# Optimization experiments

Measured on AMD Instinct MI355X. Metric: run time of the kernel, lower is better.

Reference implementation:

```python
import jax, jax.numpy as jnp
import numpy as np

N_NODES = 50000
N_EDGES = 600000
IN_C = 128
OUT_C = 128
N_REL = 8


def setup_inputs() -> dict:
    key = jax.random.key(0)
    k1, k2, k3, k4 = jax.random.split(key, 4)
    x = jax.random.normal(k1, (N_NODES, IN_C), dtype=jnp.float32)
    edge_index = jax.random.randint(k2, (2, N_EDGES), 0, N_NODES, dtype=jnp.int64)
    edge_type = jax.random.randint(k3, (N_EDGES,), 0, N_REL, dtype=jnp.int64)
    weight = jax.random.normal(k4, (N_REL, IN_C, OUT_C), dtype=jnp.float32)
    bias = jnp.zeros((OUT_C,), dtype=jnp.float32)
    return {"x": x, "edge_index": edge_index, "edge_type": edge_type,
            "weight": weight, "bias": bias}


def reference(x, edge_index, edge_type, weight, bias):
    # x: [N, in], edge_index: [2, E] (src, dst), edge_type: [E]
    # weight: [R, in, out], bias: [out]
    N = x.shape[0]
    src = edge_index[0]
    dst = edge_index[1]
    out = jnp.zeros((N, weight.shape[2]), dtype=x.dtype)
    for r in range(weight.shape[0]):
        rel_mask = (edge_type == r).astype(x.dtype)  # [E]
        transformed = x @ weight[r]                  # [N, out]
        msgs = transformed[src] * rel_mask[:, None]  # [E, out]
        sums = jax.ops.segment_sum(msgs, dst, num_segments=N)        # [N, out]
        counts = jax.ops.segment_sum(rel_mask, dst, num_segments=N)  # [N]
        mean = jnp.where(counts[:, None] > 0,
                         sums / jnp.maximum(counts, 1.0)[:, None],
                         0.0)
        out = out + mean
    return out + bias
```

## Files before the change

### kernel.cpp

```cpp
#include <hip/hip_runtime.h>
#include <hip/hip_bf16.h>


#define C128 128
#define BR 16

typedef __attribute__((ext_vector_type(8))) short short8;
typedef __attribute__((ext_vector_type(4))) float f32x4;

__device__ __forceinline__ float bf16u_f32(unsigned short u) {
    union { unsigned int i; float f; } c;
    c.i = ((unsigned int)u) << 16;
    return c.f;
}


__global__ __launch_bounds__(256) void pre_kernel(const int* __restrict__ ei,
                                                  const int* __restrict__ et,
                                                  unsigned* __restrict__ cursor,
                                                  const float* __restrict__ W,
                                                  __hip_bfloat16* __restrict__ WbT,
                                                  const float* __restrict__ x,
                                                  __hip_bfloat16* __restrict__ xb,
                                                  int n_edges, int n_nodes,
                                                  int hblk, int wblk, int wtot, int xt8) {
    int bid = blockIdx.x;
    if (bid < hblk) {
        int e = bid * 256 + threadIdx.x;
        if (e < n_edges)
            atomicAdd(&cursor[(size_t)et[e] * n_nodes + ei[n_edges + e]], 1u);
    } else if (bid < hblk + wblk) {
        int i = (bid - hblk) * 256 + threadIdx.x;
        if (i < wtot) {
            int r = i >> 14, k = (i >> 7) & 127, n = i & 127;
            int kt = k >> 5, cg = (k >> 3) & 3, j = k & 7;
            int nt = n >> 4, l16 = n & 15;
            int pos = ((((r * 4 + kt) * 8 + nt) * 4 + cg) * 16 + l16) * 8 + j;
            WbT[pos] = __float2bfloat16(W[i]);
        }
    } else {
        int i = (bid - hblk - wblk) * 256 + threadIdx.x;
        if (i < xt8) {
            const float4* src = reinterpret_cast<const float4*>(x + (size_t)i * 8);
            float4 v0 = src[0], v1 = src[1];
            short8 o;
            o[0] = (short)__bfloat16_as_ushort(__float2bfloat16(v0.x));
            o[1] = (short)__bfloat16_as_ushort(__float2bfloat16(v0.y));
            o[2] = (short)__bfloat16_as_ushort(__float2bfloat16(v0.z));
            o[3] = (short)__bfloat16_as_ushort(__float2bfloat16(v0.w));
            o[4] = (short)__bfloat16_as_ushort(__float2bfloat16(v1.x));
            o[5] = (short)__bfloat16_as_ushort(__float2bfloat16(v1.y));
            o[6] = (short)__bfloat16_as_ushort(__float2bfloat16(v1.z));
            o[7] = (short)__bfloat16_as_ushort(__float2bfloat16(v1.w));
            *reinterpret_cast<short8*>(reinterpret_cast<unsigned short*>(xb) + (size_t)i * 8) = o;
        }
    }
}


__global__ __launch_bounds__(256) void scan1_kernel(const unsigned* __restrict__ cnt,
                                                    unsigned* __restrict__ part, int total) {
    __shared__ unsigned s[256];
    int t = threadIdx.x;
    int base = blockIdx.x * 1024 + t * 4;
    unsigned sum = 0;
#pragma unroll
    for (int i = 0; i < 4; ++i) {
        int idx = base + i;
        if (idx < total) sum += cnt[idx];
    }
    s[t] = sum;
    __syncthreads();
    for (int d = 128; d > 0; d >>= 1) {
        if (t < d) s[t] += s[t + d];
        __syncthreads();
    }
    if (t == 0) part[blockIdx.x] = s[0];
}

__global__ __launch_bounds__(256) void scan23_kernel(unsigned* __restrict__ cursor,
                                                     unsigned* __restrict__ off,
                                                     const unsigned* __restrict__ part,
                                                     int total, int n_edges) {
    __shared__ unsigned s[256];
    const int t = threadIdx.x;
    const int bid = blockIdx.x;

    unsigned basesum = 0;
    for (int i0 = 0; i0 < bid; i0 += 256) {
        int i = i0 + t;
        s[t] = (i < bid) ? part[i] : 0u;
        __syncthreads();
        for (int d = 128; d > 0; d >>= 1) {
            if (t < d) s[t] += s[t + d];
            __syncthreads();
        }
        basesum += s[0];
        __syncthreads();
    }

    int base = bid * 1024 + t * 4;
    unsigned v[4];
    unsigned tsum = 0;
#pragma unroll
    for (int i = 0; i < 4; ++i) {
        int idx = base + i;
        v[i] = (idx < total) ? cursor[idx] : 0u;
        tsum += v[i];
    }
    s[t] = tsum;
    __syncthreads();
    for (int d = 1; d < 256; d <<= 1) {
        unsigned u = (t >= d) ? s[t - d] : 0u;
        __syncthreads();
        s[t] += u;
        __syncthreads();
    }
    unsigned run = s[t] - tsum + basesum;
#pragma unroll
    for (int i = 0; i < 4; ++i) {
        int idx = base + i;
        if (idx < total) {
            off[idx] = run;
            cursor[idx] = run;
            run += v[i];
        }
    }
    if (bid == 0 && t == 0) off[total] = (unsigned)n_edges;
}

__global__ __launch_bounds__(256) void place_kernel(const int* __restrict__ ei,
                                                    const int* __restrict__ et,
                                                    unsigned* __restrict__ cursor,
                                                    int* __restrict__ sorted_src,
                                                    int n_edges, int n_nodes) {
    int e = blockIdx.x * 256 + threadIdx.x;
    if (e < n_edges) {
        int src = ei[e];
        int dst = ei[n_edges + e];
        int key = et[e] * n_nodes + dst;
        unsigned pos = atomicAdd(&cursor[key], 1u);
        sorted_src[pos] = src;
    }
}


__global__ __launch_bounds__(64, 3) void fused_kernel(
    const __hip_bfloat16* __restrict__ xb, const int* __restrict__ ss,
    const unsigned* __restrict__ off, const __hip_bfloat16* __restrict__ WbT,
    const float* __restrict__ bias, float* __restrict__ out,
    int n_nodes, int n_rel) {
    const int lane = threadIdx.x & 63;
    const int l16 = lane & 15, cg = lane >> 4;
    const int row0 = blockIdx.x * BR;
    const int node = row0 + l16;
    const bool live = (node < n_nodes);
    const unsigned short* xbu = reinterpret_cast<const unsigned short*>(xb);
    const unsigned short* wpu = reinterpret_cast<const unsigned short*>(WbT);

    f32x4 acc[8];
#pragma unroll
    for (int i = 0; i < 8; ++i) acc[i] = (f32x4){0.f, 0.f, 0.f, 0.f};

    unsigned b = 0, e = 0;
    if (live) { b = off[node]; e = off[node + 1]; }

    for (int p = 0; p < n_rel; ++p) {
        unsigned nb = 0, ne = 0;
        if (p + 1 < n_rel && live) {
            size_t k = (size_t)(p + 1) * n_nodes + node;
            nb = off[k];
            ne = off[k + 1];
        }

        float a[4][8];
#pragma unroll
        for (int kt = 0; kt < 4; ++kt)
#pragma unroll
            for (int j = 0; j < 8; ++j) a[kt][j] = 0.f;

        int n0 = (int)(e - b);
        int eb = (int)b;
        int s0 = (n0 > 0) ? ss[eb] : 0;
        for (int i = 0; i < n0; ++i) {
            int sv = s0;
            s0 = (i + 1 < n0) ? ss[eb + i + 1] : 0;
            const unsigned short* rp = xbu + ((size_t)sv << 7) + cg * 8;
            short8 v0 = *reinterpret_cast<const short8*>(rp);
            short8 v1 = *reinterpret_cast<const short8*>(rp + 32);
            short8 v2 = *reinterpret_cast<const short8*>(rp + 64);
            short8 v3 = *reinterpret_cast<const short8*>(rp + 96);
#pragma unroll
            for (int j = 0; j < 8; ++j) {
                a[0][j] += bf16u_f32((unsigned short)v0[j]);
                a[1][j] += bf16u_f32((unsigned short)v1[j]);
                a[2][j] += bf16u_f32((unsigned short)v2[j]);
                a[3][j] += bf16u_f32((unsigned short)v3[j]);
            }
        }
        float inv = (n0 > 0) ? 1.0f / (float)n0 : 0.0f;
        short8 af[4];
#pragma unroll
        for (int kt = 0; kt < 4; ++kt) {
            short8 o;
#pragma unroll
            for (int j = 0; j < 8; ++j)
                o[j] = (short)__bfloat16_as_ushort(__float2bfloat16(a[kt][j] * inv));
            af[kt] = o;
        }

#pragma unroll
        for (int kt = 0; kt < 4; ++kt) {
            short8 bf[8];
#pragma unroll
            for (int nt = 0; nt < 8; ++nt)
                bf[nt] = *reinterpret_cast<const short8*>(
                    wpu + ((size_t)(((p * 4 + kt) * 8 + nt) * 64 + lane)) * 8);
#pragma unroll
            for (int nt = 0; nt < 8; ++nt)
                acc[nt] = __builtin_amdgcn_mfma_f32_16x16x32_bf16(af[kt], bf[nt],
                                                                  acc[nt], 0, 0, 0);
        }

        b = nb;
        e = ne;
    }

    const int rbase = row0 + (cg << 2);
#pragma unroll
    for (int nt = 0; nt < 8; ++nt) {
        int col = nt * 16 + l16;
        float bv = bias[col];
#pragma unroll
        for (int i = 0; i < 4; ++i) {
            int r = rbase + i;
            if (r < n_nodes)
                out[(size_t)r * C128 + col] = acc[nt][i] + bv;
        }
    }
}


static inline char* align16p(char* p) {
    return (char*)(((uintptr_t)p + 15) & ~(uintptr_t)15);
}

extern "C" void kernel_launch(void* const* d_in, const int* in_sizes, int n_in,
                              void* d_out, int out_size, void* d_ws, size_t ws_size,
                              hipStream_t stream) {
    const float* x    = (const float*)d_in[0];
    const int*   ei   = (const int*)d_in[1];
    const int*   et   = (const int*)d_in[2];
    const float* W    = (const float*)d_in[3];
    const float* bias = (const float*)d_in[4];
    float* out = (float*)d_out;

    const int n_nodes = in_sizes[0] / C128;
    const int n_edges = in_sizes[2];
    const int n_rel   = in_sizes[3] / (C128 * C128);
    const int RN = n_rel * n_nodes;

    char* p = (char*)d_ws;
    unsigned* off = (unsigned*)p;      p += (size_t)(RN + 1) * 4; p = align16p(p);
    unsigned* cursor = (unsigned*)p;   p += (size_t)RN * 4;       p = align16p(p);
    unsigned* part = (unsigned*)p;     p += 4096 * 4;
    int* sorted_src = (int*)p;         p += (size_t)n_edges * 4;  p = align16p(p);
    __hip_bfloat16* WbT = (__hip_bfloat16*)p; p += (size_t)n_rel * C128 * C128 * 2; p = align16p(p);
    __hip_bfloat16* xb = (__hip_bfloat16*)p;

    hipMemsetAsync(cursor, 0, (size_t)RN * 4, stream);

    int wtot = n_rel * C128 * C128;
    int xt8 = n_nodes * (C128 / 8);
    int hblk = (n_edges + 255) / 256;
    int wblk = (wtot + 255) / 256;
    int xblk = (xt8 + 255) / 256;
    pre_kernel<<<hblk + wblk + xblk, 256, 0, stream>>>(ei, et, cursor, W, WbT, x, xb,
                                                       n_edges, n_nodes, hblk, wblk, wtot, xt8);

    int nblk = (RN + 1023) / 1024;
    scan1_kernel<<<nblk, 256, 0, stream>>>(cursor, part, RN);
    scan23_kernel<<<nblk, 256, 0, stream>>>(cursor, off, part, RN, n_edges);
    place_kernel<<<(n_edges + 255) / 256, 256, 0, stream>>>(ei, et, cursor, sorted_src,
                                                            n_edges, n_nodes);

    int mblk = (n_nodes + BR - 1) / BR;
    fused_kernel<<<mblk, 64, 0, stream>>>(xb, sorted_src, off, WbT, bias, out,
                                          n_nodes, n_rel);
}
```

Baseline: 150.0 us.

## Split relations across four waves per block and reduce partial outputs in LDS

```diff
diff --git a/kernel.cpp b/kernel.cpp
--- a/kernel.cpp
+++ b/kernel.cpp
@@ -145,12 +145,13 @@
 }
 
 
-__global__ __launch_bounds__(64, 3) void fused_kernel(
+__global__ __launch_bounds__(256, 4) void fused_kernel(
     const __hip_bfloat16* __restrict__ xb, const int* __restrict__ ss,
     const unsigned* __restrict__ off, const __hip_bfloat16* __restrict__ WbT,
     const float* __restrict__ bias, float* __restrict__ out,
     int n_nodes, int n_rel) {
-    const int lane = threadIdx.x & 63;
+    __shared__ __align__(16) f32x4 sred[8][256];
+    const int t = threadIdx.x, lane = t & 63, w = t >> 6;
     const int l16 = lane & 15, cg = lane >> 4;
     const int row0 = blockIdx.x * BR;
     const int node = row0 + l16;
@@ -162,15 +163,13 @@
 #pragma unroll
     for (int i = 0; i < 8; ++i) acc[i] = (f32x4){0.f, 0.f, 0.f, 0.f};
 
-    unsigned b = 0, e = 0;
-    if (live) { b = off[node]; e = off[node + 1]; }
-
-    for (int p = 0; p < n_rel; ++p) {
-        unsigned nb = 0, ne = 0;
-        if (p + 1 < n_rel && live) {
-            size_t k = (size_t)(p + 1) * n_nodes + node;
-            nb = off[k];
-            ne = off[k + 1];
+    const int p_end = (w * 2 + 2 < n_rel) ? (w * 2 + 2) : n_rel;
+    for (int p = w * 2; p < p_end; ++p) {
+        unsigned b = 0, e = 0;
+        if (live) {
+            size_t k = (size_t)p * n_nodes + node;
+            b = off[k];
+            e = off[k + 1];
         }
 
         float a[4][8];
@@ -221,21 +220,26 @@
                 acc[nt] = __builtin_amdgcn_mfma_f32_16x16x32_bf16(af[kt], bf[nt],
                                                                   acc[nt], 0, 0, 0);
         }
-
-        b = nb;
-        e = ne;
-    }
-
-    const int rbase = row0 + (cg << 2);
-#pragma unroll
-    for (int nt = 0; nt < 8; ++nt) {
+    }
+
+#pragma unroll
+    for (int nt = 0; nt < 8; ++nt) sred[nt][t] = acc[nt];
+    __syncthreads();
+
+#pragma unroll
+    for (int q = 0; q < 2; ++q) {
+        int nt = w * 2 + q;
+        f32x4 r = sred[nt][lane];
+        r += sred[nt][64 + lane];
+        r += sred[nt][128 + lane];
+        r += sred[nt][192 + lane];
         int col = nt * 16 + l16;
         float bv = bias[col];
 #pragma unroll
         for (int i = 0; i < 4; ++i) {
-            int r = rbase + i;
-            if (r < n_nodes)
-                out[(size_t)r * C128 + col] = acc[nt][i] + bv;
+            int rrow = row0 + (cg << 2) + i;
+            if (rrow < n_nodes)
+                out[(size_t)rrow * C128 + col] = r[i] + bv;
         }
     }
 }
@@ -285,6 +289,6 @@
                                                             n_edges, n_nodes);
 
     int mblk = (n_nodes + BR - 1) / BR;
-    fused_kernel<<<mblk, 64, 0, stream>>>(xb, sorted_src, off, WbT, bias, out,
-                                          n_nodes, n_rel);
-}
+    fused_kernel<<<mblk, 256, 0, stream>>>(xb, sorted_src, off, WbT, bias, out,
+                                           n_nodes, n_rel);
+}
```

Result: slower. 153.8 us (+2.6%).
